# Kernel tuning notes

Measured on AMD Instinct MI355X. Metric: run time of the kernel, lower is better.

Reference implementation:

```python
import jax, jax.numpy as jnp
import numpy as np

B, T, C, H, L = 1024, 20, 512, 8, 8
V, BS = 2, 32
D = C // H
EPS = 1e-5


def setup_inputs() -> dict:
    key = jax.random.key(0)
    ks = iter(jax.random.split(key, 16))
    n = lambda shape, s=0.02: jax.random.normal(next(ks), shape, dtype=jnp.float32) * s
    return {
        "x": jax.random.normal(next(ks), (B, T, V), dtype=jnp.float32),
        "enc_w": n((V, C)), "enc_b": jnp.zeros((C,), jnp.float32),
        "wpe": n((BS, C)),
        "ln1_w": jnp.ones((L, C), jnp.float32), "ln1_b": jnp.zeros((L, C), jnp.float32),
        "attn_w": n((L, C, 3 * C)), "attn_b": jnp.zeros((L, 3 * C), jnp.float32),
        "proj_w": n((L, C, C), 0.02 / np.sqrt(2 * L)), "proj_b": jnp.zeros((L, C), jnp.float32),
        "ln2_w": jnp.ones((L, C), jnp.float32), "ln2_b": jnp.zeros((L, C), jnp.float32),
        "fc1_w": n((L, C, 4 * C)), "fc1_b": jnp.zeros((L, 4 * C), jnp.float32),
        "fc2_w": n((L, 4 * C, C), 0.02 / np.sqrt(2 * L)), "fc2_b": jnp.zeros((L, C), jnp.float32),
        "lnf_w": jnp.ones((C,), jnp.float32), "lnf_b": jnp.zeros((C,), jnp.float32),
        "pred_w": n((C, V)), "pred_b": jnp.zeros((V,), jnp.float32),
    }


def _ln(x, w, b):
    mu = x.mean(-1, keepdims=True)
    var = x.var(-1, keepdims=True)  # biased, matches torch LayerNorm
    return (x - mu) * jax.lax.rsqrt(var + EPS) * w + b


def _forward(x, enc_w, enc_b, wpe, ln1_w, ln1_b, attn_w, attn_b, proj_w, proj_b,
             ln2_w, ln2_b, fc1_w, fc1_b, fc2_w, fc2_b, lnf_w, lnf_b, pred_w, pred_b):
    # traj_encoder_1 + positional embeddings (pos = arange(1, T+1), T != 9)
    h = x @ enc_w + enc_b + wpe[1:T + 1]
    mask = jnp.tril(jnp.ones((T, T), bool))  # causal mask
    scale = 1.0 / np.sqrt(D)

    def block(h, p):
        l1w, l1b, aw, ab, pw, pb, l2w, l2b, f1w, f1b, f2w, f2b = p
        qkv = _ln(h, l1w, l1b) @ aw + ab          # [B,T,3C]
        q, k, v = jnp.split(qkv, 3, axis=-1)
        q = q.reshape(B, T, H, D).transpose(0, 2, 1, 3)
        k = k.reshape(B, T, H, D).transpose(0, 2, 1, 3)
        v = v.reshape(B, T, H, D).transpose(0, 2, 1, 3)
        att = jnp.einsum('bhqd,bhkd->bhqk', q, k) * scale
        att = jnp.where(mask, att, -jnp.inf)
        att = jax.nn.softmax(att, axis=-1)
        y = jnp.einsum('bhqk,bhkd->bhqd', att, v)
        y = y.transpose(0, 2, 1, 3).reshape(B, T, C)
        h = h + y @ pw + pb
        m = _ln(h, l2w, l2b)
        h = h + jax.nn.gelu(m @ f1w + f1b, approximate=False) @ f2w + f2b
        return h, None

    params = (ln1_w, ln1_b, attn_w, attn_b, proj_w, proj_b,
              ln2_w, ln2_b, fc1_w, fc1_b, fc2_w, fc2_b)
    h, _ = jax.lax.scan(block, h, params)
    feat = _ln(h, lnf_w, lnf_b)
    return feat @ pred_w + pred_b  # predictor_1 -> [B,T,2]


def reference(x, enc_w, enc_b, wpe, ln1_w, ln1_b, attn_w, attn_b, proj_w, proj_b,
              ln2_w, ln2_b, fc1_w, fc1_b, fc2_w, fc2_b, lnf_w, lnf_b, pred_w, pred_b):
    return _forward(x, enc_w, enc_b, wpe, ln1_w, ln1_b, attn_w, attn_b, proj_w, proj_b,
                    ln2_w, ln2_b, fc1_w, fc1_b, fc2_w, fc2_b, lnf_w, lnf_b, pred_w, pred_b)
```

## Files before the change

kernel.cpp:

```cpp
#include <hip/hip_runtime.h>
#include <hip/hip_bf16.h>
#include <math.h>

#define NB 1024
#define NT 20
#define NC 512
#define NH 8
#define NL 8
#define MTOK (NB*NT)

using bf16 = __hip_bfloat16;
typedef float f32x4 __attribute__((ext_vector_type(4)));
typedef short s16x8 __attribute__((ext_vector_type(8)));

static __device__ __forceinline__ float us2f(unsigned short u) {
    union { float f; unsigned int i; } c; c.i = ((unsigned int)u) << 16; return c.f;
}
static __device__ __forceinline__ unsigned short f2bfu(float x) {
    union { bf16 b; unsigned short u; } c; c.b = __float2bfloat16(x); return c.u;
}
static __device__ __forceinline__ bf16 f2bf(float x) { return __float2bfloat16(x); }

static __device__ __forceinline__ void cp16(const bf16* g, bf16* lds_base, int lane) {
#if __has_builtin(__builtin_amdgcn_global_load_lds)
    __builtin_amdgcn_global_load_lds(
        (const __attribute__((address_space(1))) unsigned int*)g,
        (__attribute__((address_space(3))) unsigned int*)lds_base, 16, 0, 0);
#else
    ((int4*)lds_base)[lane] = *(const int4*)g;
#endif
}

static __device__ __forceinline__ void sync_sched() {
#if __has_builtin(__builtin_amdgcn_sched_barrier)
    __builtin_amdgcn_sched_barrier(0);
#endif
}

static __device__ __forceinline__ float gelu_f(float v) {
    return v * __builtin_amdgcn_rcpf(
        1.0f + __expf(-1.5957691f * v * (1.0f + 0.044715f * v * v)));
}

__global__ __launch_bounds__(256) void enc_kernel(
    const float* __restrict__ x, const float* __restrict__ ew,
    const float* __restrict__ eb, const float* __restrict__ wpe,
    float* __restrict__ h) {
    int idx = blockIdx.x * 256 + threadIdx.x;
    int token = idx >> 7, c4 = idx & 127;
    int t = token % NT;
    float x0 = x[(size_t)token * 2], x1 = x[(size_t)token * 2 + 1];
    const float4* w4 = (const float4*)ew;
    float4 w0 = w4[c4], w1 = w4[128 + c4];
    float4 b = ((const float4*)eb)[c4];
    float4 pe = ((const float4*)(wpe + (size_t)(t + 1) * NC))[c4];
    float4 o;
    o.x = x0 * w0.x + x1 * w1.x + b.x + pe.x;
    o.y = x0 * w0.y + x1 * w1.y + b.y + pe.y;
    o.z = x0 * w0.z + x1 * w1.z + b.z + pe.z;
    o.w = x0 * w0.w + x1 * w1.w + b.w + pe.w;
    ((float4*)h)[idx] = o;
}

__global__ __launch_bounds__(256) void wconv_kernel(
    const float* __restrict__ in, bf16* __restrict__ out, int K, int N) {
    __shared__ float tile[32][33];
    int z = blockIdx.z;
    int k0 = blockIdx.x * 32, n0 = blockIdx.y * 32;
    int tx = threadIdx.x & 31, ty = threadIdx.x >> 5;
    const float* src = in + (size_t)z * K * N;
    bf16* dst = out + (size_t)z * K * N;
#pragma unroll
    for (int i = 0; i < 4; ++i)
        tile[ty + i * 8][tx] = src[(size_t)(k0 + ty + i * 8) * N + n0 + tx];
    __syncthreads();
#pragma unroll
    for (int i = 0; i < 4; ++i)
        dst[(size_t)(n0 + ty + i * 8) * K + k0 + tx] = f2bf(tile[tx][ty + i * 8]);
}

__global__ __launch_bounds__(256) void ln_kernel(
    const float* __restrict__ h, const float* __restrict__ w,
    const float* __restrict__ b, bf16* __restrict__ out) {
    int lane = threadIdx.x & 63, wave = threadIdx.x >> 6;
    int token = blockIdx.x * 4 + wave;
    const float4* row = (const float4*)(h + (size_t)token * NC);
    float4 v0 = row[lane], v1 = row[lane + 64];
    float s  = v0.x + v0.y + v0.z + v0.w + v1.x + v1.y + v1.z + v1.w;
    float sq = v0.x*v0.x + v0.y*v0.y + v0.z*v0.z + v0.w*v0.w
             + v1.x*v1.x + v1.y*v1.y + v1.z*v1.z + v1.w*v1.w;
#pragma unroll
    for (int off = 32; off; off >>= 1) {
        s  += __shfl_xor(s, off, 64);
        sq += __shfl_xor(sq, off, 64);
    }
    float mean = s * (1.0f / NC);
    float var = sq * (1.0f / NC) - mean * mean;
    float rstd = rsqrtf(var + 1e-5f);
    const float4* w4 = (const float4*)w;
    const float4* b4 = (const float4*)b;
    float4 wa = w4[lane], wb = w4[lane + 64];
    float4 ba = b4[lane], bb = b4[lane + 64];
    ushort4 o0, o1;
    o0.x = f2bfu((v0.x - mean) * rstd * wa.x + ba.x);
    o0.y = f2bfu((v0.y - mean) * rstd * wa.y + ba.y);
    o0.z = f2bfu((v0.z - mean) * rstd * wa.z + ba.z);
    o0.w = f2bfu((v0.w - mean) * rstd * wa.w + ba.w);
    o1.x = f2bfu((v1.x - mean) * rstd * wb.x + bb.x);
    o1.y = f2bfu((v1.y - mean) * rstd * wb.y + bb.y);
    o1.z = f2bfu((v1.z - mean) * rstd * wb.z + bb.z);
    o1.w = f2bfu((v1.w - mean) * rstd * wb.w + bb.w);
    *(ushort4*)(out + (size_t)token * NC + lane * 4) = o0;
    *(ushort4*)(out + (size_t)token * NC + 256 + lane * 4) = o1;
}

template <int EPI>
__global__ __launch_bounds__(256) void gemm(
    const bf16* __restrict__ A, const bf16* __restrict__ Wt,
    const float* __restrict__ bias, float* __restrict__ resid_out,
    bf16* __restrict__ outb, int N, int K) {
    __shared__ __align__(16) bf16 lA[2][128 * 32];
    __shared__ __align__(16) bf16 lB[2][128 * 32];
    const int tid = threadIdx.x;
    const int lane = tid & 63;
    const int wave = tid >> 6;
    const int wm = wave >> 1, wn = wave & 1;

    const int flat = blockIdx.y * gridDim.x + blockIdx.x;
    const int per = (gridDim.x * gridDim.y) >> 3;
    const int nid = (flat & 7) * per + (flat >> 3);
    const int mt = nid / gridDim.x;
    const int nt = nid - mt * gridDim.x;
    const int m0 = mt * 128, n0 = nt * 128;

    f32x4 acc[4][4] = {};

    const int c0 = tid, c1 = tid + 256;
    const int r0 = c0 >> 2, q0 = (((c0 & 3) ^ ((r0 >> 1) & 3)) * 8);
    const int r1 = c1 >> 2, q1 = (((c1 & 3) ^ ((r1 >> 1) & 3)) * 8);
    const bf16* Ab = A + (size_t)m0 * K;
    const bf16* Bb = Wt + (size_t)n0 * K;

    const int fm = lane & 15;
    const int fk = (((lane >> 4) ^ ((fm >> 1) & 3)) * 8);
    const int iters = K / 32;

    auto stage = [&](int kk, int buf) {
        cp16(Ab + (size_t)r0 * K + kk + q0, &lA[buf][(wave * 64) * 8], lane);
        cp16(Ab + (size_t)r1 * K + kk + q1, &lA[buf][(256 + wave * 64) * 8], lane);
        cp16(Bb + (size_t)r0 * K + kk + q0, &lB[buf][(wave * 64) * 8], lane);
        cp16(Bb + (size_t)r1 * K + kk + q1, &lB[buf][(256 + wave * 64) * 8], lane);
    };
    stage(0, 0);
    for (int it = 0; it < iters; ++it) {
        const int cur = it & 1;
        const int kn = (it + 1 < iters) ? (it + 1) * 32 : 0;
        __builtin_amdgcn_s_barrier();
        stage(kn, cur ^ 1);
        __builtin_amdgcn_s_waitcnt(0xF74);
        __builtin_amdgcn_s_barrier();
        sync_sched();

        s16x8 af[4], bfr[4];
#pragma unroll
        for (int mi = 0; mi < 4; ++mi)
            af[mi] = *(const s16x8*)&lA[cur][(wm * 64 + mi * 16 + fm) * 32 + fk];
#pragma unroll
        for (int ni = 0; ni < 4; ++ni)
            bfr[ni] = *(const s16x8*)&lB[cur][(wn * 64 + ni * 16 + fm) * 32 + fk];
#pragma unroll
        for (int mi = 0; mi < 4; ++mi)
#pragma unroll
            for (int ni = 0; ni < 4; ++ni)
                acc[mi][ni] = __builtin_amdgcn_mfma_f32_16x16x32_bf16(
                    af[mi], bfr[ni], acc[mi][ni], 0, 0, 0);
    }

    const int er = lane >> 4;
    const int ec = lane & 15;
#pragma unroll
    for (int mi = 0; mi < 4; ++mi) {
#pragma unroll
        for (int ni = 0; ni < 4; ++ni) {
            int col = n0 + wn * 64 + ni * 16 + ec;
            float bcol = bias[col];
#pragma unroll
            for (int r = 0; r < 4; ++r) {
                int row = m0 + wm * 64 + mi * 16 + er * 4 + r;
                float v = acc[mi][ni][r] + bcol;
                size_t idx = (size_t)row * N + col;
                if (EPI == 0) {
                    outb[idx] = f2bf(v);
                } else if (EPI == 1) {
                    resid_out[idx] += v;
                } else {
                    outb[idx] = f2bf(gelu_f(v));
                }
            }
        }
    }
}

template <int EPI>
__global__ __launch_bounds__(256) void gemm64(
    const bf16* __restrict__ A, const bf16* __restrict__ Wt,
    const float* __restrict__ bias, float* __restrict__ resid_out,
    bf16* __restrict__ outb, int N, int K) {
    __shared__ __align__(16) bf16 lA[2][128 * 32];
    __shared__ __align__(16) bf16 lB[2][64 * 32];
    const int tid = threadIdx.x;
    const int lane = tid & 63;
    const int wave = tid >> 6;

    const int flat = blockIdx.y * gridDim.x + blockIdx.x;
    const int per = (gridDim.x * gridDim.y) >> 3;
    const int nid = (flat & 7) * per + (flat >> 3);
    const int mt = nid / gridDim.x;
    const int nt = nid - mt * gridDim.x;
    const int m0 = mt * 128, n0 = nt * 64;

    f32x4 acc[2][4] = {};

    const int c0 = tid, c1 = tid + 256;
    const int r0 = c0 >> 2, q0 = (((c0 & 3) ^ ((r0 >> 1) & 3)) * 8);
    const int r1 = c1 >> 2, q1 = (((c1 & 3) ^ ((r1 >> 1) & 3)) * 8);
    const bf16* Ab = A + (size_t)m0 * K;
    const bf16* Bb = Wt + (size_t)n0 * K;

    const int fm = lane & 15;
    const int fk = (((lane >> 4) ^ ((fm >> 1) & 3)) * 8);
    const int iters = K / 32;

    auto stage = [&](int kk, int buf) {
        cp16(Ab + (size_t)r0 * K + kk + q0, &lA[buf][(wave * 64) * 8], lane);
        cp16(Ab + (size_t)r1 * K + kk + q1, &lA[buf][(256 + wave * 64) * 8], lane);
        cp16(Bb + (size_t)r0 * K + kk + q0, &lB[buf][(wave * 64) * 8], lane);
    };
    stage(0, 0);
    for (int it = 0; it < iters; ++it) {
        const int cur = it & 1;
        const int kn = (it + 1 < iters) ? (it + 1) * 32 : 0;
        __builtin_amdgcn_s_barrier();
        stage(kn, cur ^ 1);
        __builtin_amdgcn_s_waitcnt(0xF73);
        __builtin_amdgcn_s_barrier();
        sync_sched();

        s16x8 af[2], bfr[4];
#pragma unroll
        for (int mi = 0; mi < 2; ++mi)
            af[mi] = *(const s16x8*)&lA[cur][(wave * 32 + mi * 16 + fm) * 32 + fk];
#pragma unroll
        for (int ni = 0; ni < 4; ++ni)
            bfr[ni] = *(const s16x8*)&lB[cur][(ni * 16 + fm) * 32 + fk];
#pragma unroll
        for (int mi = 0; mi < 2; ++mi)
#pragma unroll
            for (int ni = 0; ni < 4; ++ni)
                acc[mi][ni] = __builtin_amdgcn_mfma_f32_16x16x32_bf16(
                    af[mi], bfr[ni], acc[mi][ni], 0, 0, 0);
    }

    const int er = lane >> 4;
    const int ec = lane & 15;
#pragma unroll
    for (int mi = 0; mi < 2; ++mi) {
#pragma unroll
        for (int ni = 0; ni < 4; ++ni) {
            int col = n0 + ni * 16 + ec;
            float bcol = bias[col];
#pragma unroll
            for (int r = 0; r < 4; ++r) {
                int row = m0 + wave * 32 + mi * 16 + er * 4 + r;
                float v = acc[mi][ni][r] + bcol;
                size_t idx = (size_t)row * N + col;
                if (EPI == 0) {
                    outb[idx] = f2bf(v);
                } else if (EPI == 1) {
                    resid_out[idx] += v;
                } else {
                    outb[idx] = f2bf(gelu_f(v));
                }
            }
        }
    }
}

__global__ __launch_bounds__(64) void attn_kernel(
    const bf16* __restrict__ qkv, bf16* __restrict__ y) {
    __shared__ __align__(16) float qs[NT][68];
    __shared__ __align__(16) float ks[NT][68];
    __shared__ float vT[64][21];
    __shared__ __align__(16) float P[NT][24];
    const int lane = threadIdx.x;
    const int b = blockIdx.x >> 3, hh = blockIdx.x & 7;
    const bf16* base = qkv + (size_t)b * NT * (3 * NC) + hh * 64;

    for (int idx = lane; idx < NT * 32; idx += 64) {
        int t = idx >> 5, d2 = (idx & 31) * 2;
        const unsigned short* p;
        p = (const unsigned short*)(base + (size_t)t * (3 * NC) + d2);
        qs[t][d2] = us2f(p[0]); qs[t][d2 + 1] = us2f(p[1]);
        p = (const unsigned short*)(base + (size_t)t * (3 * NC) + NC + d2);
        ks[t][d2] = us2f(p[0]); ks[t][d2 + 1] = us2f(p[1]);
        p = (const unsigned short*)(base + (size_t)t * (3 * NC) + 2 * NC + d2);
        vT[d2][t] = us2f(p[0]); vT[d2 + 1][t] = us2f(p[1]);
    }
    __syncthreads();

    for (int pp = lane; pp < NT * NT; pp += 64) {
        int i = (int)(((unsigned)pp * 52429u) >> 20);
        int j = pp - i * 20;
        const float4* qi = (const float4*)qs[i];
        const float4* kj = (const float4*)ks[j];
        float s = 0.0f;
#pragma unroll
        for (int d4 = 0; d4 < 16; ++d4) {
            float4 a = qi[d4], c = kj[d4];
            s += a.x * c.x + a.y * c.y + a.z * c.z + a.w * c.w;
        }
        P[i][j] = s * 0.125f;
    }
    __syncthreads();

    if (lane < NT) {
        int i = lane;
        float m = -INFINITY;
        for (int j = 0; j <= i; ++j) m = fmaxf(m, P[i][j]);
        float sum = 0.0f;
        for (int j = 0; j <= i; ++j) { float e = __expf(P[i][j] - m); P[i][j] = e; sum += e; }
        float inv = 1.0f / sum;
        for (int j = 0; j <= i; ++j) P[i][j] *= inv;
        for (int j = i + 1; j < NT; ++j) P[i][j] = 0.0f;
    }
    __syncthreads();

    float vr[NT];
#pragma unroll
    for (int j = 0; j < NT; ++j) vr[j] = vT[lane][j];
    bf16* yb = y + (size_t)b * NT * NC + hh * 64;
#pragma unroll
    for (int i = 0; i < NT; ++i) {
        const float4* pr = (const float4*)P[i];
        float o = 0.0f;
#pragma unroll
        for (int j4 = 0; j4 < 5; ++j4) {
            float4 pv = pr[j4];
            o += pv.x * vr[j4 * 4] + pv.y * vr[j4 * 4 + 1]
               + pv.z * vr[j4 * 4 + 2] + pv.w * vr[j4 * 4 + 3];
        }
        yb[(size_t)i * NC + lane] = f2bf(o);
    }
}

__global__ __launch_bounds__(256) void lnf_pred_kernel(
    const float* __restrict__ h, const float* __restrict__ w,
    const float* __restrict__ b, const float* __restrict__ pw,
    const float* __restrict__ pb, float* __restrict__ out) {
    int lane = threadIdx.x & 63, wave = threadIdx.x >> 6;
    int token = blockIdx.x * 4 + wave;
    const float4* row = (const float4*)(h + (size_t)token * NC);
    float4 v0 = row[lane], v1 = row[lane + 64];
    float s  = v0.x + v0.y + v0.z + v0.w + v1.x + v1.y + v1.z + v1.w;
    float sq = v0.x*v0.x + v0.y*v0.y + v0.z*v0.z + v0.w*v0.w
             + v1.x*v1.x + v1.y*v1.y + v1.z*v1.z + v1.w*v1.w;
#pragma unroll
    for (int off = 32; off; off >>= 1) {
        s  += __shfl_xor(s, off, 64);
        sq += __shfl_xor(sq, off, 64);
    }
    float mean = s * (1.0f / NC);
    float var = sq * (1.0f / NC) - mean * mean;
    float rstd = rsqrtf(var + 1e-5f);
    const float4* w4 = (const float4*)w;
    const float4* b4 = (const float4*)b;
    float4 wa = w4[lane], wb = w4[lane + 64];
    float4 ba = b4[lane], bb = b4[lane + 64];
    const float2* pw2 = (const float2*)pw;
    float a0 = 0.0f, a1 = 0.0f;
    int c = lane * 4;
    float f; float2 pv;
    f = (v0.x - mean) * rstd * wa.x + ba.x; pv = pw2[c + 0]; a0 += f * pv.x; a1 += f * pv.y;
    f = (v0.y - mean) * rstd * wa.y + ba.y; pv = pw2[c + 1]; a0 += f * pv.x; a1 += f * pv.y;
    f = (v0.z - mean) * rstd * wa.z + ba.z; pv = pw2[c + 2]; a0 += f * pv.x; a1 += f * pv.y;
    f = (v0.w - mean) * rstd * wa.w + ba.w; pv = pw2[c + 3]; a0 += f * pv.x; a1 += f * pv.y;
    c = 256 + lane * 4;
    f = (v1.x - mean) * rstd * wb.x + bb.x; pv = pw2[c + 0]; a0 += f * pv.x; a1 += f * pv.y;
    f = (v1.y - mean) * rstd * wb.y + bb.y; pv = pw2[c + 1]; a0 += f * pv.x; a1 += f * pv.y;
    f = (v1.z - mean) * rstd * wb.z + bb.z; pv = pw2[c + 2]; a0 += f * pv.x; a1 += f * pv.y;
    f = (v1.w - mean) * rstd * wb.w + bb.w; pv = pw2[c + 3]; a0 += f * pv.x; a1 += f * pv.y;
#pragma unroll
    for (int off = 32; off; off >>= 1) {
        a0 += __shfl_xor(a0, off, 64);
        a1 += __shfl_xor(a1, off, 64);
    }
    if (lane == 0) {
        out[(size_t)token * 2]     = a0 + pb[0];
        out[(size_t)token * 2 + 1] = a1 + pb[1];
    }
}

extern "C" void kernel_launch(void* const* d_in, const int* in_sizes, int n_in,
                              void* d_out, int out_size, void* d_ws, size_t ws_size,
                              hipStream_t stream) {
    (void)in_sizes; (void)n_in; (void)out_size; (void)ws_size;
    const float* x      = (const float*)d_in[0];
    const float* enc_w  = (const float*)d_in[1];
    const float* enc_b  = (const float*)d_in[2];
    const float* wpe    = (const float*)d_in[3];
    const float* ln1_w  = (const float*)d_in[4];
    const float* ln1_b  = (const float*)d_in[5];
    const float* attn_w = (const float*)d_in[6];
    const float* attn_b = (const float*)d_in[7];
    const float* proj_w = (const float*)d_in[8];
    const float* proj_b = (const float*)d_in[9];
    const float* ln2_w  = (const float*)d_in[10];
    const float* ln2_b  = (const float*)d_in[11];
    const float* fc1_w  = (const float*)d_in[12];
    const float* fc1_b  = (const float*)d_in[13];
    const float* fc2_w  = (const float*)d_in[14];
    const float* fc2_b  = (const float*)d_in[15];
    const float* lnf_w  = (const float*)d_in[16];
    const float* lnf_b  = (const float*)d_in[17];
    const float* pred_w = (const float*)d_in[18];
    const float* pred_b = (const float*)d_in[19];
    float* out = (float*)d_out;

    char* p = (char*)d_ws;
    float* h  = (float*)p;  p += (size_t)MTOK * NC * 4;
    bf16* xa  = (bf16*)p;   p += (size_t)MTOK * NC * 2;
    bf16* big = (bf16*)p;   p += (size_t)MTOK * (4 * NC) * 2;
    bf16* aT  = (bf16*)p;   p += (size_t)NL * (3 * NC) * NC * 2;
    bf16* pT  = (bf16*)p;   p += (size_t)NL * NC * NC * 2;
    bf16* f1T = (bf16*)p;   p += (size_t)NL * (4 * NC) * NC * 2;
    bf16* f2T = (bf16*)p;   p += (size_t)NL * NC * (4 * NC) * 2;

    enc_kernel<<<MTOK * 128 / 256, 256, 0, stream>>>(x, enc_w, enc_b, wpe, h);
    wconv_kernel<<<dim3(16, 48, NL), 256, 0, stream>>>(attn_w, aT, NC, 3 * NC);
    wconv_kernel<<<dim3(16, 16, NL), 256, 0, stream>>>(proj_w, pT, NC, NC);
    wconv_kernel<<<dim3(16, 64, NL), 256, 0, stream>>>(fc1_w, f1T, NC, 4 * NC);
    wconv_kernel<<<dim3(64, 16, NL), 256, 0, stream>>>(fc2_w, f2T, 4 * NC, NC);

    for (int l = 0; l < NL; ++l) {
        ln_kernel<<<MTOK / 4, 256, 0, stream>>>(h, ln1_w + l * NC, ln1_b + l * NC, xa);
        gemm<0><<<dim3(12, 160), 256, 0, stream>>>(
            xa, aT + (size_t)l * 3 * NC * NC, attn_b + l * 3 * NC, nullptr, big, 3 * NC, NC);
        attn_kernel<<<NB * NH, 64, 0, stream>>>(big, xa);
        gemm64<1><<<dim3(8, 160), 256, 0, stream>>>(
            xa, pT + (size_t)l * NC * NC, proj_b + l * NC, h, nullptr, NC, NC);
        ln_kernel<<<MTOK / 4, 256, 0, stream>>>(h, ln2_w + l * NC, ln2_b + l * NC, xa);
        gemm<2><<<dim3(16, 160), 256, 0, stream>>>(
            xa, f1T + (size_t)l * 4 * NC * NC, fc1_b + l * 4 * NC, nullptr, big, 4 * NC, NC);
        gemm64<1><<<dim3(8, 160), 256, 0, stream>>>(
            big, f2T + (size_t)l * NC * 4 * NC, fc2_b + l * NC, h, nullptr, NC, 4 * NC);
    }
    lnf_pred_kernel<<<MTOK / 4, 256, 0, stream>>>(h, lnf_w, lnf_b, pred_w, pred_b, out);
}
```

Measured before the change: 2.539 ms.

## Load GEMM A operand directly to registers and fuse residual add into LayerNorm

The GEMM kernels stop staging the A (activation) tile through LDS. Each wave now loads its own 32 rows straight from global memory into registers, prefetching one k-step ahead, while only the weight tile is double-buffered in LDS. The projection and fc2 GEMMs no longer do a read-modify-write of the fp32 residual. They write a bf16 delta that a new fused add+LayerNorm kernel, and the final LN, accumulates into h. This cuts LDS traffic and fp32 residual round-trips, but the A loads become uncoalesced 16-byte per-lane reads with no reuse across waves, and the residual delta is rounded to bf16.

```diff
diff --git a/kernel.cpp b/kernel.cpp
--- a/kernel.cpp
+++ b/kernel.cpp
@@ -114,17 +114,55 @@
     *(ushort4*)(out + (size_t)token * NC + 256 + lane * 4) = o1;
 }
 
+__global__ __launch_bounds__(256) void addln_kernel(
+    float* __restrict__ h, const bf16* __restrict__ delta,
+    const float* __restrict__ w, const float* __restrict__ b,
+    bf16* __restrict__ out) {
+    int lane = threadIdx.x & 63, wave = threadIdx.x >> 6;
+    int token = blockIdx.x * 4 + wave;
+    float4* row = (float4*)(h + (size_t)token * NC);
+    float4 v0 = row[lane], v1 = row[lane + 64];
+    const ushort4* drow = (const ushort4*)(delta + (size_t)token * NC);
+    ushort4 d0 = drow[lane], d1 = drow[lane + 64];
+    v0.x += us2f(d0.x); v0.y += us2f(d0.y); v0.z += us2f(d0.z); v0.w += us2f(d0.w);
+    v1.x += us2f(d1.x); v1.y += us2f(d1.y); v1.z += us2f(d1.z); v1.w += us2f(d1.w);
+    row[lane] = v0; row[lane + 64] = v1;
+    float s  = v0.x + v0.y + v0.z + v0.w + v1.x + v1.y + v1.z + v1.w;
+    float sq = v0.x*v0.x + v0.y*v0.y + v0.z*v0.z + v0.w*v0.w
+             + v1.x*v1.x + v1.y*v1.y + v1.z*v1.z + v1.w*v1.w;
+#pragma unroll
+    for (int off = 32; off; off >>= 1) {
+        s  += __shfl_xor(s, off, 64);
+        sq += __shfl_xor(sq, off, 64);
+    }
+    float mean = s * (1.0f / NC);
+    float var = sq * (1.0f / NC) - mean * mean;
+    float rstd = rsqrtf(var + 1e-5f);
+    const float4* w4 = (const float4*)w;
+    const float4* b4 = (const float4*)b;
+    float4 wa = w4[lane], wb = w4[lane + 64];
+    float4 ba = b4[lane], bb = b4[lane + 64];
+    ushort4 o0, o1;
+    o0.x = f2bfu((v0.x - mean) * rstd * wa.x + ba.x);
+    o0.y = f2bfu((v0.y - mean) * rstd * wa.y + ba.y);
+    o0.z = f2bfu((v0.z - mean) * rstd * wa.z + ba.z);
+    o0.w = f2bfu((v0.w - mean) * rstd * wa.w + ba.w);
+    o1.x = f2bfu((v1.x - mean) * rstd * wb.x + bb.x);
+    o1.y = f2bfu((v1.y - mean) * rstd * wb.y + bb.y);
+    o1.z = f2bfu((v1.z - mean) * rstd * wb.z + bb.z);
+    o1.w = f2bfu((v1.w - mean) * rstd * wb.w + bb.w);
+    *(ushort4*)(out + (size_t)token * NC + lane * 4) = o0;
+    *(ushort4*)(out + (size_t)token * NC + 256 + lane * 4) = o1;
+}
+
 template <int EPI>
-__global__ __launch_bounds__(256) void gemm(
+__global__ __launch_bounds__(256) void gemm_a(
     const bf16* __restrict__ A, const bf16* __restrict__ Wt,
-    const float* __restrict__ bias, float* __restrict__ resid_out,
-    bf16* __restrict__ outb, int N, int K) {
-    __shared__ __align__(16) bf16 lA[2][128 * 32];
+    const float* __restrict__ bias, bf16* __restrict__ outb, int N, int K) {
     __shared__ __align__(16) bf16 lB[2][128 * 32];
     const int tid = threadIdx.x;
     const int lane = tid & 63;
     const int wave = tid >> 6;
-    const int wm = wave >> 1, wn = wave & 1;
 
     const int flat = blockIdx.y * gridDim.x + blockIdx.x;
     const int per = (gridDim.x * gridDim.y) >> 3;
@@ -133,80 +171,76 @@
     const int nt = nid - mt * gridDim.x;
     const int m0 = mt * 128, n0 = nt * 128;
 
-    f32x4 acc[4][4] = {};
+    f32x4 acc[2][8] = {};
 
     const int c0 = tid, c1 = tid + 256;
     const int r0 = c0 >> 2, q0 = (((c0 & 3) ^ ((r0 >> 1) & 3)) * 8);
     const int r1 = c1 >> 2, q1 = (((c1 & 3) ^ ((r1 >> 1) & 3)) * 8);
-    const bf16* Ab = A + (size_t)m0 * K;
     const bf16* Bb = Wt + (size_t)n0 * K;
 
     const int fm = lane & 15;
-    const int fk = (((lane >> 4) ^ ((fm >> 1) & 3)) * 8);
+    const int fk8 = (lane >> 4) * 8;
+    const int fkS = (((lane >> 4) ^ ((fm >> 1) & 3)) * 8);
     const int iters = K / 32;
 
-    auto stage = [&](int kk, int buf) {
-        cp16(Ab + (size_t)r0 * K + kk + q0, &lA[buf][(wave * 64) * 8], lane);
-        cp16(Ab + (size_t)r1 * K + kk + q1, &lA[buf][(256 + wave * 64) * 8], lane);
+    const bf16* Arow0 = A + (size_t)(m0 + wave * 32 + fm) * K + fk8;
+    const bf16* Arow1 = Arow0 + (size_t)16 * K;
+
+    auto stageB = [&](int kk, int buf) {
         cp16(Bb + (size_t)r0 * K + kk + q0, &lB[buf][(wave * 64) * 8], lane);
         cp16(Bb + (size_t)r1 * K + kk + q1, &lB[buf][(256 + wave * 64) * 8], lane);
     };
-    stage(0, 0);
+    s16x8 a0 = *(const s16x8*)Arow0;
+    s16x8 a1 = *(const s16x8*)Arow1;
+    stageB(0, 0);
     for (int it = 0; it < iters; ++it) {
         const int cur = it & 1;
         const int kn = (it + 1 < iters) ? (it + 1) * 32 : 0;
         __builtin_amdgcn_s_barrier();
-        stage(kn, cur ^ 1);
+        s16x8 an0 = *(const s16x8*)(Arow0 + kn);
+        s16x8 an1 = *(const s16x8*)(Arow1 + kn);
+        stageB(kn, cur ^ 1);
+        sync_sched();
         __builtin_amdgcn_s_waitcnt(0xF74);
         __builtin_amdgcn_s_barrier();
         sync_sched();
 
-        s16x8 af[4], bfr[4];
-#pragma unroll
-        for (int mi = 0; mi < 4; ++mi)
-            af[mi] = *(const s16x8*)&lA[cur][(wm * 64 + mi * 16 + fm) * 32 + fk];
-#pragma unroll
-        for (int ni = 0; ni < 4; ++ni)
-            bfr[ni] = *(const s16x8*)&lB[cur][(wn * 64 + ni * 16 + fm) * 32 + fk];
-#pragma unroll
-        for (int mi = 0; mi < 4; ++mi)
-#pragma unroll
-            for (int ni = 0; ni < 4; ++ni)
-                acc[mi][ni] = __builtin_amdgcn_mfma_f32_16x16x32_bf16(
-                    af[mi], bfr[ni], acc[mi][ni], 0, 0, 0);
+        s16x8 bfr[8];
+#pragma unroll
+        for (int ni = 0; ni < 8; ++ni)
+            bfr[ni] = *(const s16x8*)&lB[cur][(ni * 16 + fm) * 32 + fkS];
+#pragma unroll
+        for (int ni = 0; ni < 8; ++ni)
+            acc[0][ni] = __builtin_amdgcn_mfma_f32_16x16x32_bf16(a0, bfr[ni], acc[0][ni], 0, 0, 0);
+#pragma unroll
+        for (int ni = 0; ni < 8; ++ni)
+            acc[1][ni] = __builtin_amdgcn_mfma_f32_16x16x32_bf16(a1, bfr[ni], acc[1][ni], 0, 0, 0);
+        a0 = an0; a1 = an1;
     }
 
     const int er = lane >> 4;
     const int ec = lane & 15;
 #pragma unroll
-    for (int mi = 0; mi < 4; ++mi) {
-#pragma unroll
-        for (int ni = 0; ni < 4; ++ni) {
-            int col = n0 + wn * 64 + ni * 16 + ec;
+    for (int mi = 0; mi < 2; ++mi) {
+#pragma unroll
+        for (int ni = 0; ni < 8; ++ni) {
+            int col = n0 + ni * 16 + ec;
             float bcol = bias[col];
 #pragma unroll
             for (int r = 0; r < 4; ++r) {
-                int row = m0 + wm * 64 + mi * 16 + er * 4 + r;
+                int row = m0 + wave * 32 + mi * 16 + er * 4 + r;
                 float v = acc[mi][ni][r] + bcol;
                 size_t idx = (size_t)row * N + col;
-                if (EPI == 0) {
-                    outb[idx] = f2bf(v);
-                } else if (EPI == 1) {
-                    resid_out[idx] += v;
-                } else {
-                    outb[idx] = f2bf(gelu_f(v));
-                }
+                if (EPI == 0) outb[idx] = f2bf(v);
+                else          outb[idx] = f2bf(gelu_f(v));
             }
         }
     }
 }
 
-template <int EPI>
-__global__ __launch_bounds__(256) void gemm64(
+__global__ __launch_bounds__(256) void gemm64_a(
     const bf16* __restrict__ A, const bf16* __restrict__ Wt,
-    const float* __restrict__ bias, float* __restrict__ resid_out,
-    bf16* __restrict__ outb, int N, int K) {
-    __shared__ __align__(16) bf16 lA[2][128 * 32];
+    const float* __restrict__ bias, bf16* __restrict__ outb, int N, int K) {
     __shared__ __align__(16) bf16 lB[2][64 * 32];
     const int tid = threadIdx.x;
     const int lane = tid & 63;
@@ -221,44 +255,47 @@
 
     f32x4 acc[2][4] = {};
 
-    const int c0 = tid, c1 = tid + 256;
+    const int c0 = tid;
     const int r0 = c0 >> 2, q0 = (((c0 & 3) ^ ((r0 >> 1) & 3)) * 8);
-    const int r1 = c1 >> 2, q1 = (((c1 & 3) ^ ((r1 >> 1) & 3)) * 8);
-    const bf16* Ab = A + (size_t)m0 * K;
     const bf16* Bb = Wt + (size_t)n0 * K;
 
     const int fm = lane & 15;
-    const int fk = (((lane >> 4) ^ ((fm >> 1) & 3)) * 8);
+    const int fk8 = (lane >> 4) * 8;
+    const int fkS = (((lane >> 4) ^ ((fm >> 1) & 3)) * 8);
     const int iters = K / 32;
 
-    auto stage = [&](int kk, int buf) {
-        cp16(Ab + (size_t)r0 * K + kk + q0, &lA[buf][(wave * 64) * 8], lane);
-        cp16(Ab + (size_t)r1 * K + kk + q1, &lA[buf][(256 + wave * 64) * 8], lane);
+    const bf16* Arow0 = A + (size_t)(m0 + wave * 32 + fm) * K + fk8;
+    const bf16* Arow1 = Arow0 + (size_t)16 * K;
+
+    auto stageB = [&](int kk, int buf) {
         cp16(Bb + (size_t)r0 * K + kk + q0, &lB[buf][(wave * 64) * 8], lane);
     };
-    stage(0, 0);
+    s16x8 a0 = *(const s16x8*)Arow0;
+    s16x8 a1 = *(const s16x8*)Arow1;
+    stageB(0, 0);
     for (int it = 0; it < iters; ++it) {
         const int cur = it & 1;
         const int kn = (it + 1 < iters) ? (it + 1) * 32 : 0;
         __builtin_amdgcn_s_barrier();
-        stage(kn, cur ^ 1);
+        s16x8 an0 = *(const s16x8*)(Arow0 + kn);
+        s16x8 an1 = *(const s16x8*)(Arow1 + kn);
+        stageB(kn, cur ^ 1);
+        sync_sched();
         __builtin_amdgcn_s_waitcnt(0xF73);
         __builtin_amdgcn_s_barrier();
         sync_sched();
 
-        s16x8 af[2], bfr[4];
-#pragma unroll
-        for (int mi = 0; mi < 2; ++mi)
-            af[mi] = *(const s16x8*)&lA[cur][(wave * 32 + mi * 16 + fm) * 32 + fk];
+        s16x8 bfr[4];
 #pragma unroll
         for (int ni = 0; ni < 4; ++ni)
-            bfr[ni] = *(const s16x8*)&lB[cur][(ni * 16 + fm) * 32 + fk];
-#pragma unroll
-        for (int mi = 0; mi < 2; ++mi)
-#pragma unroll
-            for (int ni = 0; ni < 4; ++ni)
-                acc[mi][ni] = __builtin_amdgcn_mfma_f32_16x16x32_bf16(
-                    af[mi], bfr[ni], acc[mi][ni], 0, 0, 0);
+            bfr[ni] = *(const s16x8*)&lB[cur][(ni * 16 + fm) * 32 + fkS];
+#pragma unroll
+        for (int ni = 0; ni < 4; ++ni)
+            acc[0][ni] = __builtin_amdgcn_mfma_f32_16x16x32_bf16(a0, bfr[ni], acc[0][ni], 0, 0, 0);
+#pragma unroll
+        for (int ni = 0; ni < 4; ++ni)
+            acc[1][ni] = __builtin_amdgcn_mfma_f32_16x16x32_bf16(a1, bfr[ni], acc[1][ni], 0, 0, 0);
+        a0 = an0; a1 = an1;
     }
 
     const int er = lane >> 4;
@@ -273,14 +310,7 @@
             for (int r = 0; r < 4; ++r) {
                 int row = m0 + wave * 32 + mi * 16 + er * 4 + r;
                 float v = acc[mi][ni][r] + bcol;
-                size_t idx = (size_t)row * N + col;
-                if (EPI == 0) {
-                    outb[idx] = f2bf(v);
-                } else if (EPI == 1) {
-                    resid_out[idx] += v;
-                } else {
-                    outb[idx] = f2bf(gelu_f(v));
-                }
+                outb[(size_t)row * N + col] = f2bf(v);
             }
         }
     }
@@ -354,13 +384,18 @@
 }
 
 __global__ __launch_bounds__(256) void lnf_pred_kernel(
-    const float* __restrict__ h, const float* __restrict__ w,
-    const float* __restrict__ b, const float* __restrict__ pw,
-    const float* __restrict__ pb, float* __restrict__ out) {
+    const float* __restrict__ h, const bf16* __restrict__ delta,
+    const float* __restrict__ w, const float* __restrict__ b,
+    const float* __restrict__ pw, const float* __restrict__ pb,
+    float* __restrict__ out) {
     int lane = threadIdx.x & 63, wave = threadIdx.x >> 6;
     int token = blockIdx.x * 4 + wave;
     const float4* row = (const float4*)(h + (size_t)token * NC);
     float4 v0 = row[lane], v1 = row[lane + 64];
+    const ushort4* drow = (const ushort4*)(delta + (size_t)token * NC);
+    ushort4 d0 = drow[lane], d1 = drow[lane + 64];
+    v0.x += us2f(d0.x); v0.y += us2f(d0.y); v0.z += us2f(d0.z); v0.w += us2f(d0.w);
+    v1.x += us2f(d1.x); v1.y += us2f(d1.y); v1.z += us2f(d1.z); v1.w += us2f(d1.w);
     float s  = v0.x + v0.y + v0.z + v0.w + v1.x + v1.y + v1.z + v1.w;
     float sq = v0.x*v0.x + v0.y*v0.y + v0.z*v0.z + v0.w*v0.w
              + v1.x*v1.x + v1.y*v1.y + v1.z*v1.z + v1.w*v1.w;
@@ -429,6 +464,7 @@
     char* p = (char*)d_ws;
     float* h  = (float*)p;  p += (size_t)MTOK * NC * 4;
     bf16* xa  = (bf16*)p;   p += (size_t)MTOK * NC * 2;
+    bf16* dl  = (bf16*)p;   p += (size_t)MTOK * NC * 2;
     bf16* big = (bf16*)p;   p += (size_t)MTOK * (4 * NC) * 2;
     bf16* aT  = (bf16*)p;   p += (size_t)NL * (3 * NC) * NC * 2;
     bf16* pT  = (bf16*)p;   p += (size_t)NL * NC * NC * 2;
@@ -442,17 +478,23 @@
     wconv_kernel<<<dim3(64, 16, NL), 256, 0, stream>>>(fc2_w, f2T, 4 * NC, NC);
 
     for (int l = 0; l < NL; ++l) {
-        ln_kernel<<<MTOK / 4, 256, 0, stream>>>(h, ln1_w + l * NC, ln1_b + l * NC, xa);
-        gemm<0><<<dim3(12, 160), 256, 0, stream>>>(
-            xa, aT + (size_t)l * 3 * NC * NC, attn_b + l * 3 * NC, nullptr, big, 3 * NC, NC);
+        if (l == 0)
+            ln_kernel<<<MTOK / 4, 256, 0, stream>>>(h, ln1_w, ln1_b, xa);
+        else
+            addln_kernel<<<MTOK / 4, 256, 0, stream>>>(
+                h, dl, ln1_w + l * NC, ln1_b + l * NC, xa);
+        gemm_a<0><<<dim3(12, 160), 256, 0, stream>>>(
+            xa, aT + (size_t)l * 3 * NC * NC, attn_b + l * 3 * NC, big, 3 * NC, NC);
         attn_kernel<<<NB * NH, 64, 0, stream>>>(big, xa);
-        gemm64<1><<<dim3(8, 160), 256, 0, stream>>>(
-            xa, pT + (size_t)l * NC * NC, proj_b + l * NC, h, nullptr, NC, NC);
-        ln_kernel<<<MTOK / 4, 256, 0, stream>>>(h, ln2_w + l * NC, ln2_b + l * NC, xa);
-        gemm<2><<<dim3(16, 160), 256, 0, stream>>>(
-            xa, f1T + (size_t)l * 4 * NC * NC, fc1_b + l * 4 * NC, nullptr, big, 4 * NC, NC);
-        gemm64<1><<<dim3(8, 160), 256, 0, stream>>>(
-            big, f2T + (size_t)l * NC * 4 * NC, fc2_b + l * NC, h, nullptr, NC, 4 * NC);
-    }
-    lnf_pred_kernel<<<MTOK / 4, 256, 0, stream>>>(h, lnf_w, lnf_b, pred_w, pred_b, out);
-}
+        gemm64_a<<<dim3(8, 160), 256, 0, stream>>>(
+            xa, pT + (size_t)l * NC * NC, proj_b + l * NC, dl, NC, NC);
+        addln_kernel<<<MTOK / 4, 256, 0, stream>>>(
+            h, dl, ln2_w + l * NC, ln2_b + l * NC, xa);
+        gemm_a<2><<<dim3(16, 160), 256, 0, stream>>>(
+            xa, f1T + (size_t)l * 4 * NC * NC, fc1_b + l * 4 * NC, big, 4 * NC, NC);
+        gemm64_a<<<dim3(8, 160), 256, 0, stream>>>(
+            big, f2T + (size_t)l * NC * 4 * NC, fc2_b + l * NC, dl, NC, 4 * NC);
+    }
+    lnf_pred_kernel<<<MTOK / 4, 256, 0, stream>>>(
+        h, dl, lnf_w, lnf_b, pred_w, pred_b, out);
+}
```

Measured after the change: 2.838 ms. 1.12x slower.
